# Kernel optimization log

Measured on AMD Instinct MI355X. Metric: run time of the kernel, lower is better.

Reference implementation:

```python
import jax, jax.numpy as jnp
import numpy as np

E = 25_600_000
N = 100_000

def setup_inputs() -> dict:
    key = jax.random.key(0)
    k1, k2, k3 = jax.random.split(key, 3)
    edge_weight = jax.random.uniform(k1, (E,), dtype=jnp.float32, minval=1e-3, maxval=1.0)
    src = jax.random.randint(k2, (E,), 0, N, dtype=jnp.int32)
    dst = jax.random.randint(k3, (E,), 0, N, dtype=jnp.int32)
    return {"edge_weight": edge_weight, "src": src, "dst": dst, "num_nodes": N}

def reference(edge_weight, src, dst, num_nodes):
    eps = 0.0
    # norm='both': out-degree weighted sum over src (reversed-graph scatter),
    # in-degree weighted sum over dst, then per-edge gather-multiply.
    out_deg = jax.ops.segment_sum(edge_weight, src, num_segments=num_nodes)  # [N]
    in_deg = jax.ops.segment_sum(edge_weight, dst, num_segments=num_nodes)   # [N]
    src_norm = jax.lax.rsqrt(out_deg + eps)  # pow(deg, -0.5)
    dst_norm = jax.lax.rsqrt(in_deg + eps)
    return src_norm[src] * dst_norm[dst] * edge_weight  # [E]
```

## Files before the change

### kernel.cpp

```cpp
#include <hip/hip_runtime.h>

#define TPB 256

typedef float ntf4 __attribute__((ext_vector_type(4)));
typedef int   nti4 __attribute__((ext_vector_type(4)));

#define SCAT_TPB 1024
#define S_RANGE  20352
#define SCAT_GRID 255

__device__ __forceinline__ unsigned xcc_id() {
    unsigned v;
    asm volatile("s_getreg_b32 %0, hwreg(HW_REG_XCC_ID)" : "=s"(v));
    return v & 7u;
}

__device__ __forceinline__ int calc_R(unsigned long long ws_bytes, int N) {
    unsigned long long ws_floats = ws_bytes / 4ull;
    unsigned long long r = ws_floats / (unsigned long long)(2 * N);
    if (r > 8ull) r = 8ull;
    if (r < 1ull) r = 1ull;
    return (int)r;
}

__global__ void ewn_zero_kernel(float* __restrict__ ws,
                                const int* __restrict__ pN,
                                unsigned long long ws_bytes) {
    int N = *pN;
    int R = calc_R(ws_bytes, N);
    long long total = (long long)R * 2 * N;
    for (long long i = blockIdx.x * (long long)blockDim.x + threadIdx.x; i < total;
         i += (long long)gridDim.x * blockDim.x) {
        ws[i] = 0.0f;
    }
}

__global__ __launch_bounds__(SCAT_TPB, 4) void ewn_scatter_kernel(
        const float* __restrict__ w,
        const int* __restrict__ src,
        const int* __restrict__ dst,
        float* __restrict__ ws,
        const int* __restrict__ pN,
        unsigned long long ws_bytes,
        int E) {
    __shared__ float h_out[S_RANGE];
    __shared__ float h_in[S_RANGE];

    const int N = *pN;
    const int R = calc_R(ws_bytes, N);

    int NR = (N + S_RANGE - 1) / S_RANGE;
    if (NR < 1) NR = 1;
    int M = (int)gridDim.x / NR;
    if (M < 1) M = 1;

    const int bid = blockIdx.x;
    if (bid >= NR * M) return;
    const int m = bid / NR;
    const int r = bid % NR;
    const int lo = r * S_RANGE;

    for (int i = threadIdx.x; i < S_RANGE; i += SCAT_TPB) {
        h_out[i] = 0.0f;
        h_in[i]  = 0.0f;
    }
    __syncthreads();

    long long stripe = (((long long)E + M - 1) / M + 3ll) & ~3ll;
    long long jstart = (long long)m * stripe;
    long long jend   = jstart + stripe;
    if (jend > E) jend = E;

    const long long STEP = (long long)SCAT_TPB * 4;

#define EWN_PROC(wv, sv, dv) do {                                                        \
        int t_;                                                                          \
        t_ = sv.x - lo; if ((unsigned)t_ < (unsigned)S_RANGE) unsafeAtomicAdd(&h_out[t_], wv.x); \
        t_ = sv.y - lo; if ((unsigned)t_ < (unsigned)S_RANGE) unsafeAtomicAdd(&h_out[t_], wv.y); \
        t_ = sv.z - lo; if ((unsigned)t_ < (unsigned)S_RANGE) unsafeAtomicAdd(&h_out[t_], wv.z); \
        t_ = sv.w - lo; if ((unsigned)t_ < (unsigned)S_RANGE) unsafeAtomicAdd(&h_out[t_], wv.w); \
        t_ = dv.x - lo; if ((unsigned)t_ < (unsigned)S_RANGE) unsafeAtomicAdd(&h_in[t_],  wv.x); \
        t_ = dv.y - lo; if ((unsigned)t_ < (unsigned)S_RANGE) unsafeAtomicAdd(&h_in[t_],  wv.y); \
        t_ = dv.z - lo; if ((unsigned)t_ < (unsigned)S_RANGE) unsafeAtomicAdd(&h_in[t_],  wv.z); \
        t_ = dv.w - lo; if ((unsigned)t_ < (unsigned)S_RANGE) unsafeAtomicAdd(&h_in[t_],  wv.w); \
    } while (0)

    long long j0 = jstart + (long long)threadIdx.x * 4;

    for (; j0 + 3 * STEP + 3 < jend; j0 += 4 * STEP) {
        float4 wv0 = *(const float4*)(w + j0);
        int4   sv0 = *(const int4*)(src + j0);
        int4   dv0 = *(const int4*)(dst + j0);
        float4 wv1 = *(const float4*)(w + j0 + STEP);
        int4   sv1 = *(const int4*)(src + j0 + STEP);
        int4   dv1 = *(const int4*)(dst + j0 + STEP);
        float4 wv2 = *(const float4*)(w + j0 + 2 * STEP);
        int4   sv2 = *(const int4*)(src + j0 + 2 * STEP);
        int4   dv2 = *(const int4*)(dst + j0 + 2 * STEP);
        float4 wv3 = *(const float4*)(w + j0 + 3 * STEP);
        int4   sv3 = *(const int4*)(src + j0 + 3 * STEP);
        int4   dv3 = *(const int4*)(dst + j0 + 3 * STEP);
        EWN_PROC(wv0, sv0, dv0);
        EWN_PROC(wv1, sv1, dv1);
        EWN_PROC(wv2, sv2, dv2);
        EWN_PROC(wv3, sv3, dv3);
    }
    for (; j0 + 3 < jend; j0 += STEP) {
        float4 wv = *(const float4*)(w + j0);
        int4   sv = *(const int4*)(src + j0);
        int4   dv = *(const int4*)(dst + j0);
        EWN_PROC(wv, sv, dv);
    }
    if (j0 < jend) {
        for (long long j = j0; j < jend; ++j) {
            float wj = w[j];
            int t;
            t = src[j] - lo; if ((unsigned)t < (unsigned)S_RANGE) unsafeAtomicAdd(&h_out[t], wj);
            t = dst[j] - lo; if ((unsigned)t < (unsigned)S_RANGE) unsafeAtomicAdd(&h_in[t],  wj);
        }
    }
#undef EWN_PROC
    __syncthreads();

    const unsigned xcc = xcc_id();
    int hi = N - lo;
    if (hi > S_RANGE) hi = S_RANGE;

    if (R == 8) {
        float* deg_out = ws + (unsigned long long)xcc * 2ull * N;
        float* deg_in  = deg_out + N;
        for (int i = threadIdx.x; i < hi; i += SCAT_TPB) {
            __hip_atomic_fetch_add(&deg_out[lo + i], h_out[i], __ATOMIC_RELAXED, __HIP_MEMORY_SCOPE_WORKGROUP);
            __hip_atomic_fetch_add(&deg_in[lo + i],  h_in[i],  __ATOMIC_RELAXED, __HIP_MEMORY_SCOPE_WORKGROUP);
        }
    } else {
        float* deg_out = ws + (unsigned long long)(xcc % (unsigned)R) * 2ull * N;
        float* deg_in  = deg_out + N;
        for (int i = threadIdx.x; i < hi; i += SCAT_TPB) {
            atomicAdd(&deg_out[lo + i], h_out[i]);
            atomicAdd(&deg_in[lo + i],  h_in[i]);
        }
    }
}

__global__ void ewn_reduce_norm_kernel(float* __restrict__ ws,
                                       const int* __restrict__ pN,
                                       unsigned long long ws_bytes) {
    int N = *pN;
    int R = calc_R(ws_bytes, N);
    long long n2 = 2ll * N;
    for (long long i = blockIdx.x * (long long)blockDim.x + threadIdx.x; i < n2;
         i += (long long)gridDim.x * blockDim.x) {
        float s = 0.0f;
        for (int r = 0; r < R; ++r) s += ws[(long long)r * n2 + i];
        ws[i] = 1.0f / sqrtf(s);
    }
}

__global__ void ewn_gather_kernel(const float* __restrict__ w,
                                  const int* __restrict__ src,
                                  const int* __restrict__ dst,
                                  const float* __restrict__ ws,
                                  const int* __restrict__ pN,
                                  float* __restrict__ out,
                                  int E) {
    const int N = *pN;
    const float* norm_out = ws;
    const float* norm_in  = ws + N;

    const long long tid  = (long long)blockIdx.x * blockDim.x + threadIdx.x;
    const long long half = (long long)gridDim.x * blockDim.x * 4;
    long long ia = tid * 4;
    long long ib = ia + half;

    if (ib + 3 < E) {
        ntf4 wva = __builtin_nontemporal_load((const ntf4*)(w + ia));
        nti4 sva = __builtin_nontemporal_load((const nti4*)(src + ia));
        nti4 dva = __builtin_nontemporal_load((const nti4*)(dst + ia));
        ntf4 wvb = __builtin_nontemporal_load((const ntf4*)(w + ib));
        nti4 svb = __builtin_nontemporal_load((const nti4*)(src + ib));
        nti4 dvb = __builtin_nontemporal_load((const nti4*)(dst + ib));
        float sa0 = norm_out[sva.x], sa1 = norm_out[sva.y], sa2 = norm_out[sva.z], sa3 = norm_out[sva.w];
        float da0 = norm_in[dva.x],  da1 = norm_in[dva.y],  da2 = norm_in[dva.z],  da3 = norm_in[dva.w];
        float sb0 = norm_out[svb.x], sb1 = norm_out[svb.y], sb2 = norm_out[svb.z], sb3 = norm_out[svb.w];
        float db0 = norm_in[dvb.x],  db1 = norm_in[dvb.y],  db2 = norm_in[dvb.z],  db3 = norm_in[dvb.w];
        ntf4 ova, ovb;
        ova.x = sa0 * da0 * wva.x;
        ova.y = sa1 * da1 * wva.y;
        ova.z = sa2 * da2 * wva.z;
        ova.w = sa3 * da3 * wva.w;
        ovb.x = sb0 * db0 * wvb.x;
        ovb.y = sb1 * db1 * wvb.y;
        ovb.z = sb2 * db2 * wvb.z;
        ovb.w = sb3 * db3 * wvb.w;
        __builtin_nontemporal_store(ova, (ntf4*)(out + ia));
        __builtin_nontemporal_store(ovb, (ntf4*)(out + ib));
    } else {
        for (int b = 0; b < 2; ++b) {
            long long i4 = b ? ib : ia;
            if (i4 + 3 < E) {
                ntf4 wv = __builtin_nontemporal_load((const ntf4*)(w + i4));
                nti4 sv = __builtin_nontemporal_load((const nti4*)(src + i4));
                nti4 dv = __builtin_nontemporal_load((const nti4*)(dst + i4));
                ntf4 ov;
                ov.x = norm_out[sv.x] * norm_in[dv.x] * wv.x;
                ov.y = norm_out[sv.y] * norm_in[dv.y] * wv.y;
                ov.z = norm_out[sv.z] * norm_in[dv.z] * wv.z;
                ov.w = norm_out[sv.w] * norm_in[dv.w] * wv.w;
                __builtin_nontemporal_store(ov, (ntf4*)(out + i4));
            } else if (i4 < E) {
                for (long long j = i4; j < E && j < i4 + 4; ++j) {
                    out[j] = norm_out[src[j]] * norm_in[dst[j]] * w[j];
                }
            }
        }
    }
}

extern "C" void kernel_launch(void* const* d_in, const int* in_sizes, int n_in,
                              void* d_out, int out_size, void* d_ws, size_t ws_size,
                              hipStream_t stream) {
    const float* edge_weight = (const float*)d_in[0];
    const int*   src         = (const int*)d_in[1];
    const int*   dst         = (const int*)d_in[2];
    const int*   pN          = (const int*)d_in[3];
    float* out = (float*)d_out;
    const int E = in_sizes[0];
    float* ws = (float*)d_ws;
    unsigned long long wsb = (unsigned long long)ws_size;

    int nBlocksGather = (int)(((long long)E / 8 + TPB - 1) / TPB);
    if (nBlocksGather < 1) nBlocksGather = 1;

    ewn_zero_kernel<<<1024, TPB, 0, stream>>>(ws, pN, wsb);
    ewn_scatter_kernel<<<SCAT_GRID, SCAT_TPB, 0, stream>>>(edge_weight, src, dst, ws, pN, wsb, E);
    ewn_reduce_norm_kernel<<<1024, TPB, 0, stream>>>(ws, pN, wsb);
    ewn_gather_kernel<<<nBlocksGather, TPB, 0, stream>>>(edge_weight, src, dst, ws, pN, out, E);
}
```

Baseline: 699.1 us.

## Split scatter into separate src/dst passes with half LDS and doubled grid

The fused scatter, which built out- and in-degree histograms in two LDS arrays, becomes one kernel launched twice, once for src and once for dst, each using a single LDS histogram. Halving LDS per block allows more resident blocks, so the grid and launch bounds are doubled. The edge weights are now read twice, and more blocks each flush a partial histogram with global atomics. sched_barrier hints are added to cluster loads ahead of atomics and gathers in both scatter and gather kernels.

```diff
diff --git a/kernel.cpp b/kernel.cpp
--- a/kernel.cpp
+++ b/kernel.cpp
@@ -7,7 +7,7 @@
 
 #define SCAT_TPB 1024
 #define S_RANGE  20352
-#define SCAT_GRID 255
+#define SCAT_GRID 510
 
 __device__ __forceinline__ unsigned xcc_id() {
     unsigned v;
@@ -35,16 +35,15 @@
     }
 }
 
-__global__ __launch_bounds__(SCAT_TPB, 4) void ewn_scatter_kernel(
+__global__ __launch_bounds__(SCAT_TPB, 8) void ewn_scatter_kernel(
         const float* __restrict__ w,
-        const int* __restrict__ src,
-        const int* __restrict__ dst,
+        const int* __restrict__ idx,
         float* __restrict__ ws,
         const int* __restrict__ pN,
         unsigned long long ws_bytes,
-        int E) {
-    __shared__ float h_out[S_RANGE];
-    __shared__ float h_in[S_RANGE];
+        int E,
+        int table_off_is_N) {
+    __shared__ float h[S_RANGE];
 
     const int N = *pN;
     const int R = calc_R(ws_bytes, N);
@@ -60,10 +59,7 @@
     const int r = bid % NR;
     const int lo = r * S_RANGE;
 
-    for (int i = threadIdx.x; i < S_RANGE; i += SCAT_TPB) {
-        h_out[i] = 0.0f;
-        h_in[i]  = 0.0f;
-    }
+    for (int i = threadIdx.x; i < S_RANGE; i += SCAT_TPB) h[i] = 0.0f;
     __syncthreads();
 
     long long stripe = (((long long)E + M - 1) / M + 3ll) & ~3ll;
@@ -73,53 +69,44 @@
 
     const long long STEP = (long long)SCAT_TPB * 4;
 
-#define EWN_PROC(wv, sv, dv) do {                                                        \
-        int t_;                                                                          \
-        t_ = sv.x - lo; if ((unsigned)t_ < (unsigned)S_RANGE) unsafeAtomicAdd(&h_out[t_], wv.x); \
-        t_ = sv.y - lo; if ((unsigned)t_ < (unsigned)S_RANGE) unsafeAtomicAdd(&h_out[t_], wv.y); \
-        t_ = sv.z - lo; if ((unsigned)t_ < (unsigned)S_RANGE) unsafeAtomicAdd(&h_out[t_], wv.z); \
-        t_ = sv.w - lo; if ((unsigned)t_ < (unsigned)S_RANGE) unsafeAtomicAdd(&h_out[t_], wv.w); \
-        t_ = dv.x - lo; if ((unsigned)t_ < (unsigned)S_RANGE) unsafeAtomicAdd(&h_in[t_],  wv.x); \
-        t_ = dv.y - lo; if ((unsigned)t_ < (unsigned)S_RANGE) unsafeAtomicAdd(&h_in[t_],  wv.y); \
-        t_ = dv.z - lo; if ((unsigned)t_ < (unsigned)S_RANGE) unsafeAtomicAdd(&h_in[t_],  wv.z); \
-        t_ = dv.w - lo; if ((unsigned)t_ < (unsigned)S_RANGE) unsafeAtomicAdd(&h_in[t_],  wv.w); \
+#define EWN_PROC1(wv, sv) do {                                                            \
+        int t_;                                                                           \
+        t_ = sv.x - lo; if ((unsigned)t_ < (unsigned)S_RANGE) unsafeAtomicAdd(&h[t_], wv.x); \
+        t_ = sv.y - lo; if ((unsigned)t_ < (unsigned)S_RANGE) unsafeAtomicAdd(&h[t_], wv.y); \
+        t_ = sv.z - lo; if ((unsigned)t_ < (unsigned)S_RANGE) unsafeAtomicAdd(&h[t_], wv.z); \
+        t_ = sv.w - lo; if ((unsigned)t_ < (unsigned)S_RANGE) unsafeAtomicAdd(&h[t_], wv.w); \
     } while (0)
 
     long long j0 = jstart + (long long)threadIdx.x * 4;
 
     for (; j0 + 3 * STEP + 3 < jend; j0 += 4 * STEP) {
         float4 wv0 = *(const float4*)(w + j0);
-        int4   sv0 = *(const int4*)(src + j0);
-        int4   dv0 = *(const int4*)(dst + j0);
+        int4   sv0 = *(const int4*)(idx + j0);
         float4 wv1 = *(const float4*)(w + j0 + STEP);
-        int4   sv1 = *(const int4*)(src + j0 + STEP);
-        int4   dv1 = *(const int4*)(dst + j0 + STEP);
+        int4   sv1 = *(const int4*)(idx + j0 + STEP);
         float4 wv2 = *(const float4*)(w + j0 + 2 * STEP);
-        int4   sv2 = *(const int4*)(src + j0 + 2 * STEP);
-        int4   dv2 = *(const int4*)(dst + j0 + 2 * STEP);
+        int4   sv2 = *(const int4*)(idx + j0 + 2 * STEP);
         float4 wv3 = *(const float4*)(w + j0 + 3 * STEP);
-        int4   sv3 = *(const int4*)(src + j0 + 3 * STEP);
-        int4   dv3 = *(const int4*)(dst + j0 + 3 * STEP);
-        EWN_PROC(wv0, sv0, dv0);
-        EWN_PROC(wv1, sv1, dv1);
-        EWN_PROC(wv2, sv2, dv2);
-        EWN_PROC(wv3, sv3, dv3);
+        int4   sv3 = *(const int4*)(idx + j0 + 3 * STEP);
+        __builtin_amdgcn_sched_barrier(0);
+        EWN_PROC1(wv0, sv0);
+        EWN_PROC1(wv1, sv1);
+        EWN_PROC1(wv2, sv2);
+        EWN_PROC1(wv3, sv3);
     }
     for (; j0 + 3 < jend; j0 += STEP) {
         float4 wv = *(const float4*)(w + j0);
-        int4   sv = *(const int4*)(src + j0);
-        int4   dv = *(const int4*)(dst + j0);
-        EWN_PROC(wv, sv, dv);
+        int4   sv = *(const int4*)(idx + j0);
+        EWN_PROC1(wv, sv);
     }
     if (j0 < jend) {
         for (long long j = j0; j < jend; ++j) {
             float wj = w[j];
-            int t;
-            t = src[j] - lo; if ((unsigned)t < (unsigned)S_RANGE) unsafeAtomicAdd(&h_out[t], wj);
-            t = dst[j] - lo; if ((unsigned)t < (unsigned)S_RANGE) unsafeAtomicAdd(&h_in[t],  wj);
-        }
-    }
-#undef EWN_PROC
+            int t = idx[j] - lo;
+            if ((unsigned)t < (unsigned)S_RANGE) unsafeAtomicAdd(&h[t], wj);
+        }
+    }
+#undef EWN_PROC1
     __syncthreads();
 
     const unsigned xcc = xcc_id();
@@ -127,18 +114,16 @@
     if (hi > S_RANGE) hi = S_RANGE;
 
     if (R == 8) {
-        float* deg_out = ws + (unsigned long long)xcc * 2ull * N;
-        float* deg_in  = deg_out + N;
+        float* deg = ws + (unsigned long long)xcc * 2ull * N
+                        + (table_off_is_N ? (unsigned long long)N : 0ull);
         for (int i = threadIdx.x; i < hi; i += SCAT_TPB) {
-            __hip_atomic_fetch_add(&deg_out[lo + i], h_out[i], __ATOMIC_RELAXED, __HIP_MEMORY_SCOPE_WORKGROUP);
-            __hip_atomic_fetch_add(&deg_in[lo + i],  h_in[i],  __ATOMIC_RELAXED, __HIP_MEMORY_SCOPE_WORKGROUP);
+            __hip_atomic_fetch_add(&deg[lo + i], h[i], __ATOMIC_RELAXED, __HIP_MEMORY_SCOPE_WORKGROUP);
         }
     } else {
-        float* deg_out = ws + (unsigned long long)(xcc % (unsigned)R) * 2ull * N;
-        float* deg_in  = deg_out + N;
+        float* deg = ws + (unsigned long long)(xcc % (unsigned)R) * 2ull * N
+                        + (table_off_is_N ? (unsigned long long)N : 0ull);
         for (int i = threadIdx.x; i < hi; i += SCAT_TPB) {
-            atomicAdd(&deg_out[lo + i], h_out[i]);
-            atomicAdd(&deg_in[lo + i],  h_in[i]);
+            atomicAdd(&deg[lo + i], h[i]);
         }
     }
 }
@@ -157,13 +142,14 @@
     }
 }
 
-__global__ void ewn_gather_kernel(const float* __restrict__ w,
-                                  const int* __restrict__ src,
-                                  const int* __restrict__ dst,
-                                  const float* __restrict__ ws,
-                                  const int* __restrict__ pN,
-                                  float* __restrict__ out,
-                                  int E) {
+__global__ __launch_bounds__(TPB, 8) void ewn_gather_kernel(
+        const float* __restrict__ w,
+        const int* __restrict__ src,
+        const int* __restrict__ dst,
+        const float* __restrict__ ws,
+        const int* __restrict__ pN,
+        float* __restrict__ out,
+        int E) {
     const int N = *pN;
     const float* norm_out = ws;
     const float* norm_in  = ws + N;
@@ -180,10 +166,12 @@
         ntf4 wvb = __builtin_nontemporal_load((const ntf4*)(w + ib));
         nti4 svb = __builtin_nontemporal_load((const nti4*)(src + ib));
         nti4 dvb = __builtin_nontemporal_load((const nti4*)(dst + ib));
+        __builtin_amdgcn_sched_barrier(0);
         float sa0 = norm_out[sva.x], sa1 = norm_out[sva.y], sa2 = norm_out[sva.z], sa3 = norm_out[sva.w];
         float da0 = norm_in[dva.x],  da1 = norm_in[dva.y],  da2 = norm_in[dva.z],  da3 = norm_in[dva.w];
         float sb0 = norm_out[svb.x], sb1 = norm_out[svb.y], sb2 = norm_out[svb.z], sb3 = norm_out[svb.w];
         float db0 = norm_in[dvb.x],  db1 = norm_in[dvb.y],  db2 = norm_in[dvb.z],  db3 = norm_in[dvb.w];
+        __builtin_amdgcn_sched_barrier(0);
         ntf4 ova, ovb;
         ova.x = sa0 * da0 * wva.x;
         ova.y = sa1 * da1 * wva.y;
@@ -233,7 +221,8 @@
     if (nBlocksGather < 1) nBlocksGather = 1;
 
     ewn_zero_kernel<<<1024, TPB, 0, stream>>>(ws, pN, wsb);
-    ewn_scatter_kernel<<<SCAT_GRID, SCAT_TPB, 0, stream>>>(edge_weight, src, dst, ws, pN, wsb, E);
+    ewn_scatter_kernel<<<SCAT_GRID, SCAT_TPB, 0, stream>>>(edge_weight, src, ws, pN, wsb, E, 0);
+    ewn_scatter_kernel<<<SCAT_GRID, SCAT_TPB, 0, stream>>>(edge_weight, dst, ws, pN, wsb, E, 1);
     ewn_reduce_norm_kernel<<<1024, TPB, 0, stream>>>(ws, pN, wsb);
     ewn_gather_kernel<<<nBlocksGather, TPB, 0, stream>>>(edge_weight, src, dst, ws, pN, out, E);
 }
```

After: 755.7 us. 1.08x slower.
